# Performance work log

Measured on AMD Instinct MI355X. Metric: run time of the kernel, lower is better.

## Reference

```python
import jax, jax.numpy as jnp
import numpy as np

N_WIRES = 4
DIM = 2 ** N_WIRES  # 16 amplitudes per 4-qubit state
# PauliZ sign table: wire 0 is the most-significant bit of the flattened index
_SIGNS = (1.0 - 2.0 * ((np.arange(DIM)[:, None] >> np.array([3, 2, 1, 0])[None, :]) & 1)).astype(np.float32)  # [16,4]


def _rx(state, theta, wire):
    """Apply RX(theta) on `wire`. state: [N,2,2,2,2] complex64; theta: [N] or scalar."""
    c = jnp.cos(theta / 2.0)
    s = -1j * jnp.sin(theta / 2.0)
    c = c.astype(jnp.complex64).reshape(c.shape + (1, 1, 1))
    s = s.astype(jnp.complex64).reshape(s.shape + (1, 1, 1))
    st = jnp.moveaxis(state, wire + 1, -1)
    a0, a1 = st[..., 0], st[..., 1]
    new = jnp.stack([c * a0 + s * a1, s * a0 + c * a1], axis=-1)
    return jnp.moveaxis(new, -1, wire + 1)


def _cnot(state, ctrl, tgt):
    s = jnp.moveaxis(state, (ctrl + 1, tgt + 1), (1, 2))
    s = jnp.stack([s[:, 0], s[:, 1, ::-1]], axis=1)
    return jnp.moveaxis(s, (1, 2), (ctrl + 1, tgt + 1))


def _simulate(angles, q_params):
    """angles: [N,4] RX encoding angles; q_params: [n_layers,4]. Returns PauliZ expvals [N,4]."""
    N = angles.shape[0]
    state = jnp.zeros((N, DIM), jnp.complex64).at[:, 0].set(1.0).reshape((N, 2, 2, 2, 2))
    for w in range(N_WIRES):                      # encoder: RX(x_w) on wire w
        state = _rx(state, angles[:, w], w)
    for l in range(q_params.shape[0]):            # variational layers
        for w in range(N_WIRES):
            state = _rx(state, q_params[l, w], w)
        for src in range(N_WIRES):                # CNOT ring (i, (i+1)%4)
            state = _cnot(state, src, (src + 1) % N_WIRES)
    probs = jnp.abs(state.reshape(N, DIM)) ** 2
    return probs @ jnp.asarray(_SIGNS)            # [N,4]


def setup_inputs() -> dict:
    key = jax.random.key(0)
    k1, k2, k3 = jax.random.split(key, 3)
    B, S, E = 8, 1024, 128
    x = jax.random.normal(k1, (B, S, E), dtype=jnp.float32)
    q_params = jax.random.normal(k2, (1, 4), dtype=jnp.float32)
    W_combine = jax.random.normal(k3, (E, E), dtype=jnp.float32) / jnp.sqrt(jnp.float32(E))
    return {"x": x, "q_params": q_params, "W_combine": W_combine}


def reference(x, q_params, W_combine):
    B, S, E = x.shape
    H, DK = 32, 4
    # quantum encoding of every (token, head) chunk -- q, k, v are identical
    angles = x.reshape(B * S * H, DK)
    qkv = _simulate(angles, q_params).reshape(B, S, H, DK)
    h = jnp.transpose(qkv, (0, 2, 1, 3))          # [B,H,S,DK]
    scores = jnp.einsum('bhqd,bhkd->bhqk', h, h) / jnp.sqrt(jnp.float32(DK))
    attn = jax.nn.softmax(scores, axis=-1)        # dropout is identity in eval
    out = jnp.einsum('bhqk,bhkd->bhqd', attn, h)
    out = jnp.transpose(out, (0, 2, 1, 3)).reshape(B, S, E)
    return out @ W_combine.T                      # combine_heads (no bias)
```

## Files before the change

kernel.cpp:

```cpp
#include <hip/hip_runtime.h>

constexpr int kS = 1024;
constexpr int NM = 126;

typedef __fp16 fp16x2 __attribute__((ext_vector_type(2)));
typedef _Float16 half4v __attribute__((ext_vector_type(4)));
typedef _Float16 half8v __attribute__((ext_vector_type(8)));
typedef float float4v __attribute__((ext_vector_type(4)));


__device__ __forceinline__ float wcoef(int a0, int a1, int a2, int a3) {
  const float b[6] = {1.0031455f, 1.0010453f, 0.4860342f,
                      0.1641117f, 0.0507286f, 0.0097257f};
  const float f[6] = {1.f, 1.f, 2.f, 6.f, 24.f, 120.f};
  const float p2[6] = {1.f, 2.f, 4.f, 8.f, 16.f, 32.f};
  int n = a0 + a1 + a2 + a3;
  return b[n] * f[n] / (p2[n] * f[a0] * f[a1] * f[a2] * f[a3]);
}

template <class F>
__device__ __forceinline__ void for_each_mono(float z0, float z1, float z2,
                                              float z3, F&& f) {
  int idx = 0;
  float p0 = 1.f;
#pragma unroll
  for (int a0 = 0; a0 <= 5; ++a0) {
    float p1 = p0;
#pragma unroll
    for (int a1 = 0; a1 <= 5 - a0; ++a1) {
      float p2 = p1;
#pragma unroll
      for (int a2 = 0; a2 <= 5 - a0 - a1; ++a2) {
        float p3 = p2;
#pragma unroll
        for (int a3 = 0; a3 <= 5 - a0 - a1 - a2; ++a3) {
          f(idx, p3, a0, a1, a2, a3);
          ++idx;
          p3 *= z3;
        }
        p2 *= z2;
      }
      p1 *= z1;
    }
    p0 *= z0;
  }
}

__global__ __launch_bounds__(256) void qenc_kernel(
    const float4* __restrict__ x4, const float* __restrict__ qp,
    uint2* __restrict__ h16u, const float* __restrict__ W,
    _Float16* __restrict__ wtb) {
  int idx = blockIdx.x * 256 + threadIdx.x;
  if (blockIdx.x < 64) {
    int i = idx;
    int col = i >> 7, e = i & 127;
    wtb[((e >> 3) << 10) + (col << 3) + (e & 7)] = (_Float16)W[i];
  }
  float4 a = x4[idx];
  float c0 = cosf(a.x + qp[0]);
  float c1 = cosf(a.y + qp[1]);
  float c2 = cosf(a.z + qp[2]);
  float c3 = cosf(a.w + qp[3]);
  float z1 = c0 * c1;
  float z2 = z1 * c2;
  float z3 = z2 * c3;
  float z0 = c1 * c2 * c3;
  union { half4v h; uint2 u; } z;
  z.h.x = (_Float16)z0;
  z.h.y = (_Float16)z1;
  z.h.z = (_Float16)z2;
  z.h.w = (_Float16)z3;
  int b = idx >> 15;
  int s = (idx >> 5) & (kS - 1);
  int head = idx & 31;
  int bh = b * 32 + head;
  h16u[(bh << 10) + s] = z.u;
}

__global__ __launch_bounds__(256) void featM_kernel(
    const _Float16* __restrict__ h16, float* __restrict__ Mpart) {
  __shared__ ushort sm[128][136];
  __shared__ ushort vvb[2048];
  const int bh = blockIdx.x >> 1;
  const int half = blockIdx.x & 1;
  const int t = threadIdx.x;
  const bool hiH = t >= 128;
  const int tok = t & 127;
  const uint2* __restrict__ hb = (const uint2*)(h16) + (bh << 10) + (half << 9);

  for (int i = t; i < 2 * 136; i += 256) sm[126 + i / 136][i % 136] = 0;
  for (int i = t; i < 2048; i += 256)
    vvb[i] = (((i >> 3) & 15) == 4) ? (ushort)0x3C00u : (ushort)0u;

  const int lane = t & 63;
  const int w = t >> 6;
  const int c = lane & 15, g = lane >> 4;
  float4v acc[2] = {};

  for (int ch = 0; ch < 4; ++ch) {
    __syncthreads();
    {
      union { uint2 u; half4v h; ushort4 us; } uz;
      uz.u = hb[(ch << 7) + tok];
      float z0 = (float)uz.h.x, z1 = (float)uz.h.y;
      float z2 = (float)uz.h.z, z3 = (float)uz.h.w;
      if (!hiH) {
        int base = ((tok >> 3) << 7) + (tok & 7);
        vvb[base + 0] = uz.us.x;
        vvb[base + 8] = uz.us.y;
        vvb[base + 16] = uz.us.z;
        vvb[base + 24] = uz.us.w;
      }
      for_each_mono(z0, z1, z2, z3,
                    [&](int mi, float m, int, int, int, int) {
                      if (hiH ? (mi >= 63) : (mi < 63)) {
                        union { _Float16 h; ushort u; } cv;
                        cv.h = (_Float16)m;
                        sm[mi][tok] = cv.u;
                      }
                    });
    }
    __syncthreads();
    {
      const uint4* __restrict__ vvb4 = (const uint4*)vvb;
      union U4H { uint4 u; half8v h; };
#pragma unroll
      for (int ks = 0; ks < 4; ++ks) {
        U4H ub;
        ub.u = vvb4[(((ks << 2) + g) << 4) + c];
#pragma unroll
        for (int tl = 0; tl < 2; ++tl) {
          const uint4* arow4 = (const uint4*)&sm[(w << 5) + (tl << 4) + c][0];
          U4H ua;
          ua.u = arow4[(ks << 2) + g];
          acc[tl] = __builtin_amdgcn_mfma_f32_16x16x32_f16(ua.h, ub.h,
                                                           acc[tl], 0, 0, 0);
        }
      }
    }
  }

  if (c < 5) {
    float* mp = Mpart + ((bh << 1) + half) * NM * 5;
#pragma unroll
    for (int tl = 0; tl < 2; ++tl) {
#pragma unroll
      for (int reg = 0; reg < 4; ++reg) {
        int row = (w << 5) + (tl << 4) + (g << 2) + reg;
        if (row < NM) mp[row * 5 + c] = acc[tl][reg];
      }
    }
  }
}

__global__ __launch_bounds__(256) void featC_kernel(
    const _Float16* __restrict__ h16, const float* __restrict__ Mpart,
    uint2* __restrict__ o16u2) {
  __shared__ float Mw[NM][8];
  const int bh = blockIdx.x >> 1;
  const int qh = blockIdx.x & 1;
  const int t = threadIdx.x;
  if (t < NM) {
    const float* m0 = Mpart + ((bh << 1) * NM + t) * 5;
    const float* m1 = m0 + NM * 5;
#pragma unroll
    for (int c = 0; c < 5; ++c) Mw[t][c] = m0[c] + m1[c];
  }
  __syncthreads();

  const int q0 = (qh << 9) + t;
  const uint2* hz = (const uint2*)h16 + (bh << 10);
  union { uint2 u; half4v h; } ua, ub;
  ua.u = hz[q0];
  ub.u = hz[q0 + 256];
  float xa0 = (float)ua.h.x, xa1 = (float)ua.h.y;
  float xa2 = (float)ua.h.z, xa3 = (float)ua.h.w;
  float xb0 = (float)ub.h.x, xb1 = (float)ub.h.y;
  float xb2 = (float)ub.h.z, xb3 = (float)ub.h.w;

  float nA0 = 0.f, nA1 = 0.f, nA2 = 0.f, nA3 = 0.f, dA = 0.f;
  float nB0 = 0.f, nB1 = 0.f, nB2 = 0.f, nB3 = 0.f, dB = 0.f;

  int idx = 0;
  float pa0 = 1.f, pb0 = 1.f;
#pragma unroll
  for (int a0 = 0; a0 <= 5; ++a0) {
    float pa1 = pa0, pb1 = pb0;
#pragma unroll
    for (int a1 = 0; a1 <= 5 - a0; ++a1) {
      float pa2 = pa1, pb2 = pb1;
#pragma unroll
      for (int a2 = 0; a2 <= 5 - a0 - a1; ++a2) {
        float pa3 = pa2, pb3 = pb2;
#pragma unroll
        for (int a3 = 0; a3 <= 5 - a0 - a1 - a2; ++a3) {
          float w = wcoef(a0, a1, a2, a3);
          float wa = pa3 * w, wb = pb3 * w;
          float4 M4 = *(const float4*)&Mw[idx][0];
          float M5 = Mw[idx][4];
          nA0 += wa * M4.x; nA1 += wa * M4.y;
          nA2 += wa * M4.z; nA3 += wa * M4.w;
          dA += wa * M5;
          nB0 += wb * M4.x; nB1 += wb * M4.y;
          nB2 += wb * M4.z; nB3 += wb * M4.w;
          dB += wb * M5;
          ++idx;
          pa3 *= xa3; pb3 *= xb3;
        }
        pa2 *= xa2; pb2 *= xb2;
      }
      pa1 *= xa1; pb1 *= xb1;
    }
    pa0 *= xa0; pb0 *= xb0;
  }

  const int b_ = bh >> 5, head = bh & 31;
  {
    float inv = 1.0f / dA;
    union { fp16x2 p[2]; uint2 u; } res;
    res.p[0] = __builtin_amdgcn_cvt_pkrtz(nA0 * inv, nA1 * inv);
    res.p[1] = __builtin_amdgcn_cvt_pkrtz(nA2 * inv, nA3 * inv);
    o16u2[(((b_ << 10) + q0) << 5) + head] = res.u;
  }
  {
    float inv = 1.0f / dB;
    union { fp16x2 p[2]; uint2 u; } res;
    res.p[0] = __builtin_amdgcn_cvt_pkrtz(nB0 * inv, nB1 * inv);
    res.p[1] = __builtin_amdgcn_cvt_pkrtz(nB2 * inv, nB3 * inv);
    o16u2[(((b_ << 10) + q0 + 256) << 5) + head] = res.u;
  }
}

__global__ __launch_bounds__(256) void combine_kernel(
    const _Float16* __restrict__ o16, const _Float16* __restrict__ wtb,
    float* __restrict__ out) {
  const int lane = threadIdx.x & 63;
  const int wv = threadIdx.x >> 6;
  const int job = blockIdx.x * 4 + wv;
  const int rt = job >> 3, ct = job & 7;
  const int c = lane & 15, g = lane >> 4;
  const uint4* a4 = (const uint4*)o16;
  const uint4* b4 = (const uint4*)wtb;
  const int arow = (rt << 4) + c;
  union U4H { uint4 u; half8v h; };
  float4v acc = {};
#pragma unroll
  for (int t = 0; t < 4; ++t) {
    U4H ua, ub;
    ua.u = a4[(arow << 4) + (t << 2) + g];
    ub.u = b4[(((t << 2) + g) << 7) + (ct << 4) + c];
    acc = __builtin_amdgcn_mfma_f32_16x16x32_f16(ua.h, ub.h, acc, 0, 0, 0);
  }
  const int orow = (rt << 4) + (g << 2);
  const int ocol = (ct << 4) + c;
#pragma unroll
  for (int reg = 0; reg < 4; ++reg)
    out[(orow + reg) * 128 + ocol] = acc[reg];
}

extern "C" void kernel_launch(void* const* d_in, const int* in_sizes, int n_in,
                              void* d_out, int out_size, void* d_ws,
                              size_t ws_size, hipStream_t stream) {
  const float* x = (const float*)d_in[0];
  const float* qp = (const float*)d_in[1];
  const float* W = (const float*)d_in[2];
  float* out = (float*)d_out;

  char* ws = (char*)d_ws;
  _Float16* h16 = (_Float16*)ws;
  float* Mpart = (float*)(ws + (2 << 20));
  _Float16* o16 = (_Float16*)(ws + (6 << 20));
  _Float16* wtb = (_Float16*)(ws + (8 << 20));

  qenc_kernel<<<1024, 256, 0, stream>>>((const float4*)x, qp, (uint2*)h16, W,
                                        wtb);
  featM_kernel<<<512, 256, 0, stream>>>(h16, Mpart);
  featC_kernel<<<512, 256, 0, stream>>>(h16, Mpart, (uint2*)o16);
  combine_kernel<<<1024, 256, 0, stream>>>(o16, wtb, out);
}
```

Baseline: 32.72 us.

## Fuse moment-accumulation and feature-combine kernels into one per-head block

Merges featM and featC into one kernel where each 512-thread block owns a whole (batch, head) and keeps the reduced moment matrix in shared memory. This removes the Mpart global round trip, the cross-half partial sum and one kernel launch. The cost is half as many blocks (256 instead of 512) with larger shared-memory tiles, so there is less parallelism to fill the GPU. Each wave now does one 16-row MFMA tile over 8 k-steps.

```diff
diff --git a/kernel.cpp b/kernel.cpp
--- a/kernel.cpp
+++ b/kernel.cpp
@@ -77,31 +77,31 @@
   h16u[(bh << 10) + s] = z.u;
 }
 
-__global__ __launch_bounds__(256) void featM_kernel(
-    const _Float16* __restrict__ h16, float* __restrict__ Mpart) {
-  __shared__ ushort sm[128][136];
-  __shared__ ushort vvb[2048];
-  const int bh = blockIdx.x >> 1;
-  const int half = blockIdx.x & 1;
+__global__ __launch_bounds__(512) void featMC_kernel(
+    const _Float16* __restrict__ h16, uint2* __restrict__ o16u2) {
+  __shared__ ushort sm[128][264];
+  __shared__ ushort vvb[4096];
+  __shared__ float Mw[NM][8];
+  const int bh = blockIdx.x;
   const int t = threadIdx.x;
-  const bool hiH = t >= 128;
-  const int tok = t & 127;
-  const uint2* __restrict__ hb = (const uint2*)(h16) + (bh << 10) + (half << 9);
-
-  for (int i = t; i < 2 * 136; i += 256) sm[126 + i / 136][i % 136] = 0;
-  for (int i = t; i < 2048; i += 256)
+  const bool hiH = t >= 256;
+  const int tok = t & 255;
+  const uint2* __restrict__ hb = (const uint2*)(h16) + (bh << 10);
+
+  for (int i = t; i < 2 * 264; i += 512) sm[126 + i / 264][i % 264] = 0;
+  for (int i = t; i < 4096; i += 512)
     vvb[i] = (((i >> 3) & 15) == 4) ? (ushort)0x3C00u : (ushort)0u;
 
   const int lane = t & 63;
   const int w = t >> 6;
   const int c = lane & 15, g = lane >> 4;
-  float4v acc[2] = {};
+  float4v acc = {};
 
   for (int ch = 0; ch < 4; ++ch) {
     __syncthreads();
     {
       union { uint2 u; half4v h; ushort4 us; } uz;
-      uz.u = hb[(ch << 7) + tok];
+      uz.u = hb[(ch << 8) + tok];
       float z0 = (float)uz.h.x, z1 = (float)uz.h.y;
       float z2 = (float)uz.h.z, z3 = (float)uz.h.w;
       if (!hiH) {
@@ -123,60 +123,35 @@
     __syncthreads();
     {
       const uint4* __restrict__ vvb4 = (const uint4*)vvb;
+      const uint4* __restrict__ arow4 = (const uint4*)&sm[(w << 4) + c][0];
       union U4H { uint4 u; half8v h; };
 #pragma unroll
-      for (int ks = 0; ks < 4; ++ks) {
-        U4H ub;
+      for (int ks = 0; ks < 8; ++ks) {
+        U4H ub, ua;
         ub.u = vvb4[(((ks << 2) + g) << 4) + c];
-#pragma unroll
-        for (int tl = 0; tl < 2; ++tl) {
-          const uint4* arow4 = (const uint4*)&sm[(w << 5) + (tl << 4) + c][0];
-          U4H ua;
-          ua.u = arow4[(ks << 2) + g];
-          acc[tl] = __builtin_amdgcn_mfma_f32_16x16x32_f16(ua.h, ub.h,
-                                                           acc[tl], 0, 0, 0);
-        }
+        ua.u = arow4[(ks << 2) + g];
+        acc = __builtin_amdgcn_mfma_f32_16x16x32_f16(ua.h, ub.h, acc, 0, 0, 0);
       }
     }
   }
 
   if (c < 5) {
-    float* mp = Mpart + ((bh << 1) + half) * NM * 5;
-#pragma unroll
-    for (int tl = 0; tl < 2; ++tl) {
-#pragma unroll
-      for (int reg = 0; reg < 4; ++reg) {
-        int row = (w << 5) + (tl << 4) + (g << 2) + reg;
-        if (row < NM) mp[row * 5 + c] = acc[tl][reg];
-      }
-    }
-  }
-}
-
-__global__ __launch_bounds__(256) void featC_kernel(
-    const _Float16* __restrict__ h16, const float* __restrict__ Mpart,
-    uint2* __restrict__ o16u2) {
-  __shared__ float Mw[NM][8];
-  const int bh = blockIdx.x >> 1;
-  const int qh = blockIdx.x & 1;
-  const int t = threadIdx.x;
-  if (t < NM) {
-    const float* m0 = Mpart + ((bh << 1) * NM + t) * 5;
-    const float* m1 = m0 + NM * 5;
-#pragma unroll
-    for (int c = 0; c < 5; ++c) Mw[t][c] = m0[c] + m1[c];
+#pragma unroll
+    for (int reg = 0; reg < 4; ++reg) {
+      int row = (w << 4) + (g << 2) + reg;
+      if (row < NM) Mw[row][c] = acc[reg];
+    }
   }
   __syncthreads();
 
-  const int q0 = (qh << 9) + t;
-  const uint2* hz = (const uint2*)h16 + (bh << 10);
-  union { uint2 u; half4v h; } ua, ub;
-  ua.u = hz[q0];
-  ub.u = hz[q0 + 256];
-  float xa0 = (float)ua.h.x, xa1 = (float)ua.h.y;
-  float xa2 = (float)ua.h.z, xa3 = (float)ua.h.w;
-  float xb0 = (float)ub.h.x, xb1 = (float)ub.h.y;
-  float xb2 = (float)ub.h.z, xb3 = (float)ub.h.w;
+  const int q0 = t;
+  union { uint2 u; half4v h; } ua_, ub_;
+  ua_.u = hb[q0];
+  ub_.u = hb[q0 + 512];
+  float xa0 = (float)ua_.h.x, xa1 = (float)ua_.h.y;
+  float xa2 = (float)ua_.h.z, xa3 = (float)ua_.h.w;
+  float xb0 = (float)ub_.h.x, xb1 = (float)ub_.h.y;
+  float xb2 = (float)ub_.h.z, xb3 = (float)ub_.h.w;
 
   float nA0 = 0.f, nA1 = 0.f, nA2 = 0.f, nA3 = 0.f, dA = 0.f;
   float nB0 = 0.f, nB1 = 0.f, nB2 = 0.f, nB3 = 0.f, dB = 0.f;
@@ -194,8 +169,8 @@
         float pa3 = pa2, pb3 = pb2;
 #pragma unroll
         for (int a3 = 0; a3 <= 5 - a0 - a1 - a2; ++a3) {
-          float w = wcoef(a0, a1, a2, a3);
-          float wa = pa3 * w, wb = pb3 * w;
+          float wc = wcoef(a0, a1, a2, a3);
+          float wa = pa3 * wc, wb = pb3 * wc;
           float4 M4 = *(const float4*)&Mw[idx][0];
           float M5 = Mw[idx][4];
           nA0 += wa * M4.x; nA1 += wa * M4.y;
@@ -227,7 +202,7 @@
     union { fp16x2 p[2]; uint2 u; } res;
     res.p[0] = __builtin_amdgcn_cvt_pkrtz(nB0 * inv, nB1 * inv);
     res.p[1] = __builtin_amdgcn_cvt_pkrtz(nB2 * inv, nB3 * inv);
-    o16u2[(((b_ << 10) + q0 + 256) << 5) + head] = res.u;
+    o16u2[(((b_ << 10) + q0 + 512) << 5) + head] = res.u;
   }
 }
 
@@ -268,13 +243,11 @@
 
   char* ws = (char*)d_ws;
   _Float16* h16 = (_Float16*)ws;
-  float* Mpart = (float*)(ws + (2 << 20));
-  _Float16* o16 = (_Float16*)(ws + (6 << 20));
-  _Float16* wtb = (_Float16*)(ws + (8 << 20));
+  _Float16* o16 = (_Float16*)(ws + (2 << 20));
+  _Float16* wtb = (_Float16*)(ws + (4 << 20));
 
   qenc_kernel<<<1024, 256, 0, stream>>>((const float4*)x, qp, (uint2*)h16, W,
                                         wtb);
-  featM_kernel<<<512, 256, 0, stream>>>(h16, Mpart);
-  featC_kernel<<<512, 256, 0, stream>>>(h16, Mpart, (uint2*)o16);
+  featMC_kernel<<<256, 512, 0, stream>>>(h16, (uint2*)o16);
   combine_kernel<<<1024, 256, 0, stream>>>(o16, wtb, out);
 }
```

Result: slower. 59.04 us (median of 2 runs) (+80.5%).
